# Kernel tuning notes

Measured on AMD Instinct MI355X. Metric: run time of the kernel, lower is better.

Reference implementation:

```python
import jax, jax.numpy as jnp
import numpy as np

N, D, H = 4096, 1024, 4096
EPS = 1e-5


def setup_inputs() -> dict:
    key = jax.random.key(0)
    ks = jax.random.split(key, 12)
    s_in = 1.0 / np.sqrt(D)
    s_hid = 1.0 / np.sqrt(H)
    return {
        "x": jax.random.normal(ks[0], (N, D), dtype=jnp.float32),
        "Wq": jax.random.uniform(ks[1], (D, H), jnp.float32, -s_in, s_in),
        "Wk": jax.random.uniform(ks[2], (D, H), jnp.float32, -s_in, s_in),
        "Wv": jax.random.uniform(ks[3], (D, H), jnp.float32, -s_in, s_in),
        "Wo": jax.random.uniform(ks[4], (H, D), jnp.float32, -s_hid, s_hid),
        "W1": jax.random.uniform(ks[5], (D, H), jnp.float32, -s_in, s_in),
        "b1": jax.random.uniform(ks[6], (H,), jnp.float32, -s_in, s_in),
        "W2": jax.random.uniform(ks[7], (H, D), jnp.float32, -s_hid, s_hid),
        "b2": jax.random.uniform(ks[8], (D,), jnp.float32, -s_hid, s_hid),
        "g1": jnp.ones((D,), jnp.float32),
        "be1": jnp.zeros((D,), jnp.float32),
        "g2": jnp.ones((D,), jnp.float32),
        "be2": jnp.zeros((D,), jnp.float32),
    }


def _layernorm(x, g, b):
    mu = jnp.mean(x, axis=-1, keepdims=True)
    var = jnp.mean(jnp.square(x - mu), axis=-1, keepdims=True)
    return (x - mu) * jax.lax.rsqrt(var + EPS) * g + b


def reference(x, Wq, Wk, Wv, Wo, W1, b1, W2, b2, g1, be1, g2, be2):
    # --- attention (single head, unscaled, as in the source) ---
    q = x @ Wq                      # [N, H]
    k = x @ Wk                      # [N, H]
    v = x @ Wv                      # [N, H]
    scores = jax.nn.softmax(q @ k.T, axis=-1)  # [N, N]
    attn = (scores @ v) @ Wo        # [N, D]
    h = _layernorm(x + attn, g1, be1)
    # --- feed-forward ---
    ff = jax.nn.relu(h @ W1 + b1) @ W2 + b2
    return _layernorm(h + ff, g2, be2)
```

## Files before the change

kernel.cpp:

```cpp
#include <hip/hip_runtime.h>
#include <hip/hip_bf16.h>

using f16 = _Float16;
typedef __attribute__((ext_vector_type(8))) f16 half8;
typedef __attribute__((ext_vector_type(4))) f16 half4;
typedef __attribute__((ext_vector_type(4))) float floatx4;

#define LN_EPS 1e-5f

__device__ __forceinline__ void gload_lds16(const f16* g, f16* l) {
  __builtin_amdgcn_global_load_lds(
      (const __attribute__((address_space(1))) void*)g,
      (__attribute__((address_space(3))) void*)l, 16, 0, 0);
}

#define CFENCE asm volatile("" ::: "memory")
#define WAIT_VM(N) asm volatile("s_waitcnt vmcnt(" #N ")" ::: "memory")
#define BARRIER()                    \
  do {                               \
    CFENCE;                          \
    __builtin_amdgcn_s_barrier();    \
    CFENCE;                          \
  } while (0)

template <int EPI>
__device__ __forceinline__ void gemm256_core(
    const f16* __restrict__ A, const f16* __restrict__ B,
    f16* __restrict__ Cz, const float* __restrict__ bias,
    int lda, int ldb, int ldc, int kper, int kbeg, int bm, int bn,
    f16* smp) {
  const int t = threadIdx.x;
  const int wave = t >> 6, lane = t & 63;
  const int wm = (wave >> 2) << 7;
  const int wn = (wave & 3) << 6;
  const int lrow = lane & 15, lkc = lane >> 4;

  const int srow = lane >> 3;
  const int schunk = ((lane & 7) ^ srow) << 3;
  const f16* Ag = A + (size_t)(bm + wave * 16 + srow) * lda + kbeg + schunk;
  const f16* Bg = B + (size_t)(bn + wave * 16 + srow) * ldb + kbeg + schunk;

  const int co0 = ((lkc ^ (lrow & 7)) << 3);
  const int co1 = (((4 + lkc) ^ (lrow & 7)) << 3);

  floatx4 acc[8][4] = {};
  half8 af[4][2];
  half8 bf[2][2][2];

  auto STAGE = [&](int b, int tt, int h) {
    if (h < 2) {
      const f16* src = Ag + (size_t)(h * 128) * lda + tt * 64;
      f16* d = smp + (b * 2) * 16384 + h * 8192 + wave * 1024;
      gload_lds16(src, d);
      gload_lds16(src + (size_t)8 * lda, d + 512);
    } else {
      const f16* src = Bg + (size_t)((h - 2) * 128) * ldb + tt * 64;
      f16* d = smp + (b * 2 + 1) * 16384 + (h - 2) * 8192 + wave * 1024;
      gload_lds16(src, d);
      gload_lds16(src + (size_t)8 * ldb, d + 512);
    }
  };
  auto LDA = [&](int b, int qm) {
    const f16* base = smp + (b * 2) * 16384 + (wm + qm * 64 + lrow) * 64;
#pragma unroll
    for (int fm = 0; fm < 4; ++fm) {
      af[fm][0] = *(const half8*)(base + fm * (16 * 64) + co0);
      af[fm][1] = *(const half8*)(base + fm * (16 * 64) + co1);
    }
  };
  auto LDB = [&](int b, int qn) {
    const f16* base = smp + (b * 2 + 1) * 16384 + (wn + qn * 32 + lrow) * 64;
#pragma unroll
    for (int fn = 0; fn < 2; ++fn) {
      bf[qn][fn][0] = *(const half8*)(base + fn * (16 * 64) + co0);
      bf[qn][fn][1] = *(const half8*)(base + fn * (16 * 64) + co1);
    }
  };
  auto MFMAQ = [&](int qm, int qn) {
    __builtin_amdgcn_s_setprio(1);
#pragma unroll
    for (int kk = 0; kk < 2; ++kk)
#pragma unroll
      for (int fm = 0; fm < 4; ++fm)
#pragma unroll
        for (int fn = 0; fn < 2; ++fn)
          acc[qm * 4 + fm][qn * 2 + fn] =
              __builtin_amdgcn_mfma_f32_16x16x32_f16(
                  af[fm][kk], bf[qn][fn][kk], acc[qm * 4 + fm][qn * 2 + fn],
                  0, 0, 0);
    __builtin_amdgcn_s_setprio(0);
  };

  const int NT = kper >> 6;
  const int NI = NT >> 1;

  STAGE(0, 0, 0); STAGE(0, 0, 1); STAGE(0, 0, 2); STAGE(0, 0, 3);
  STAGE(1, 1, 0);
  WAIT_VM(2);
  BARRIER();

  for (int i = 0; i < NI; ++i) {
    const bool last = (i == NI - 1);
    const int tb = 2 * i;
    LDA(0, 0); LDB(0, 0); STAGE(1, tb + 1, 1);
    BARRIER(); MFMAQ(0, 0); BARRIER();
    LDB(0, 1); STAGE(1, tb + 1, 2);
    BARRIER(); MFMAQ(0, 1); BARRIER();
    LDA(0, 1); STAGE(1, tb + 1, 3);
    BARRIER(); MFMAQ(1, 0); BARRIER();
    if (!last) {
      STAGE(0, tb + 2, 0);
      WAIT_VM(2);
    } else {
      WAIT_VM(0);
    }
    BARRIER(); MFMAQ(1, 1); BARRIER();
    LDA(1, 0); LDB(1, 0);
    if (!last) STAGE(0, tb + 2, 1);
    BARRIER(); MFMAQ(0, 0); BARRIER();
    LDB(1, 1);
    if (!last) STAGE(0, tb + 2, 2);
    BARRIER(); MFMAQ(0, 1); BARRIER();
    LDA(1, 1);
    if (!last) STAGE(0, tb + 2, 3);
    BARRIER(); MFMAQ(1, 0); BARRIER();
    if (!last) {
      STAGE(1, tb + 3, 0);
      WAIT_VM(2);
    }
    BARRIER(); MFMAQ(1, 1); BARRIER();
  }

  const int crow0 = bm + wm + lkc * 4;
  const int ccol0 = bn + wn + lrow;
#pragma unroll
  for (int i = 0; i < 8; ++i) {
#pragma unroll
    for (int r2 = 0; r2 < 4; ++r2) {
      const size_t row = (size_t)(crow0 + i * 16 + r2);
#pragma unroll
      for (int j = 0; j < 4; ++j) {
        const int col = ccol0 + j * 16;
        float v = acc[i][j][r2];
        if (EPI == 2) v = fmaxf(v + bias[col], 0.0f);
        Cz[row * (size_t)ldc + col] = (f16)v;
      }
    }
  }
}

__device__ __forceinline__ int xcd_swizzle(int id, int nwg) {
  const int q = nwg >> 3, r = nwg & 7;
  const int xcd = id & 7, lin = id >> 3;
  return (xcd < r ? xcd * (q + 1) : r * (q + 1) + (xcd - r) * q) + lin;
}

template <int EPI>
__global__ __launch_bounds__(512, 2) void gemm_nt256(
    const f16* __restrict__ A, const f16* __restrict__ B,
    f16* __restrict__ Ch, const float* __restrict__ bias,
    int M, int Nc, int K, int lda, int ldb, int ldc) {
  __shared__ f16 sm[4][256 * 64];
  const int gx = gridDim.x, gy = gridDim.y;
  const int nwg = gx * gy * gridDim.z;
  const int id = blockIdx.x + gx * (blockIdx.y + gy * blockIdx.z);
  const int nid = xcd_swizzle(id, nwg);
  const int bx = nid % gx;
  const int by = (nid / gx) % gy;
  const int bz = nid / (gx * gy);
  const int kper = K / gridDim.z;
  gemm256_core<EPI>(A, B, Ch + (size_t)bz * M * ldc, bias, lda, ldb, ldc,
                    kper, bz * kper, by << 8, bx << 8, &sm[0][0]);
}

__global__ __launch_bounds__(512, 2) void gemm_pre256(
    const f16* __restrict__ Wkb, const f16* __restrict__ Wqb,
    const f16* __restrict__ WoT, const f16* __restrict__ Wvb,
    f16* __restrict__ parQK, f16* __restrict__ parVO, int D, int H) {
  __shared__ f16 sm[4][256 * 64];
  const int id = blockIdx.x + 4 * (blockIdx.y + 4 * blockIdx.z);
  const int nid = xcd_swizzle(id, 256);
  const int bx = nid & 3, by = (nid >> 2) & 3, z = nid >> 4;
  const int zz = z & 7;
  const f16* A = (z < 8) ? Wkb : WoT;
  const f16* B = (z < 8) ? Wqb : Wvb;
  f16* slab = ((z < 8) ? parQK : parVO) + (size_t)zz * D * D;
  gemm256_core<1>(A, B, slab, nullptr, H, H, D, H / 8, zz * (H / 8),
                  by << 8, bx << 8, &sm[0][0]);
}

__global__ __launch_bounds__(512, 2) void gemm_dual256(
    const f16* __restrict__ xb, const f16* __restrict__ WqkT,
    const f16* __restrict__ WvoT, f16* __restrict__ th,
    f16* __restrict__ xvoT, int N, int D) {
  __shared__ f16 sm[4][256 * 64];
  const int id = blockIdx.x + 4 * blockIdx.y;
  const int nid = xcd_swizzle(id, 128);
  const int bx = nid & 3, y = nid >> 2;
  if (y < 16)
    gemm256_core<1>(xb, WqkT, th, nullptr, D, D, D, D, 0,
                    y << 8, bx << 8, &sm[0][0]);
  else
    gemm256_core<1>(WvoT, xb, xvoT, nullptr, D, D, N, D, 0,
                    bx << 8, (y - 16) << 8, &sm[0][0]);
}

__global__ void prep_inputs(const float* x, const float* Wq, const float* Wk,
                            const float* Wv, const float* W1, const float* Wo,
                            const float* W2, f16* xb, f16* Wqb, f16* Wkb,
                            f16* Wvb, f16* W1T, f16* WoT, f16* W2T) {
  const int z = blockIdx.y;
  const int b = blockIdx.x;
  const int t = threadIdx.x;
  if (z >= 3) {
    const float* in = (z == 3) ? x : (z == 4) ? Wq : (z == 5) ? Wk : Wv;
    f16* out = (z == 3) ? xb : (z == 4) ? Wqb : (z == 5) ? Wkb : Wvb;
    const size_t i = ((size_t)b * 256 + t) * 16;
    const float4 a0 = *(const float4*)(in + i);
    const float4 a1 = *(const float4*)(in + i + 4);
    const float4 a2 = *(const float4*)(in + i + 8);
    const float4 a3 = *(const float4*)(in + i + 12);
    half8 v0 = {(f16)a0.x, (f16)a0.y, (f16)a0.z, (f16)a0.w,
                (f16)a1.x, (f16)a1.y, (f16)a1.z, (f16)a1.w};
    half8 v1 = {(f16)a2.x, (f16)a2.y, (f16)a2.z, (f16)a2.w,
                (f16)a3.x, (f16)a3.y, (f16)a3.z, (f16)a3.w};
    *(half8*)(out + i) = v0;
    *(half8*)(out + i + 8) = v1;
    return;
  }
  int R, C, tx, ty;
  const float* in;
  f16* out;
  if (z == 0) {
    R = 1024; C = 4096; in = W1; out = W1T;
    tx = b & 63; ty = b >> 6;
  } else {
    R = 4096; C = 1024; in = (z == 1) ? Wo : W2;
    out = (z == 1) ? WoT : W2T;
    tx = b & 15; ty = b >> 4;
  }
  const int r0 = ty << 6, c0 = tx << 6;
  __shared__ f16 lt[64 * 64];
  const int lr = t >> 4;
  const int lc = t & 15;
  const int q3 = lr & 3;
  const int rb = lr & ~3;
  const int myc = lc * 4 + q3;
#pragma unroll
  for (int rr = 0; rr < 4; ++rr) {
    const int r = lr + rr * 16;
    const float4 f = *(const float4*)(in + (size_t)(r0 + r) * C + c0 + lc * 4);
    float v0 = f.x, v1 = f.y, v2 = f.z, v3 = f.w;
    {
      const bool hi = (q3 & 2) != 0;
      float sA = hi ? v0 : v2;
      float sB = hi ? v1 : v3;
      sA = __shfl_xor(sA, 32);
      sB = __shfl_xor(sB, 32);
      if (hi) { v0 = sA; v1 = sB; } else { v2 = sA; v3 = sB; }
    }
    {
      const bool od = (q3 & 1) != 0;
      float sC = od ? v0 : v1;
      float sD = od ? v2 : v3;
      sC = __shfl_xor(sC, 16);
      sD = __shfl_xor(sD, 16);
      if (od) { v0 = sC; v2 = sD; } else { v1 = sC; v3 = sD; }
    }
    half4 hv = {(f16)v0, (f16)v1, (f16)v2, (f16)v3};
    const int rbase = rb + rr * 16;
    *(half4*)(lt + myc * 64 + (rbase ^ ((myc & 15) << 2))) = hv;
  }
  __syncthreads();
  const int oc = t >> 3, orr = (t & 7) << 3;
#pragma unroll
  for (int cc = 0; cc < 2; ++cc) {
    const int c = oc + cc * 32;
    const int swz = (c & 15) << 2;
    const half4 ha = *(const half4*)(lt + c * 64 + (orr ^ swz));
    const half4 hb4 = *(const half4*)(lt + c * 64 + ((orr + 4) ^ swz));
    half8 v = {ha[0], ha[1], ha[2], ha[3], hb4[0], hb4[1], hb4[2], hb4[3]};
    *(half8*)(out + (size_t)(c0 + c) * R + r0 + orr) = v;
  }
}

__global__ void reduce_dual(const f16* __restrict__ parQK,
                            const f16* __restrict__ parVO,
                            f16* __restrict__ WqkT, f16* __restrict__ WvoT,
                            int n) {
  const int half = gridDim.x >> 1;
  const bool second = blockIdx.x >= half;
  const f16* par = second ? parVO : parQK;
  f16* out = second ? WvoT : WqkT;
  const int b = second ? blockIdx.x - half : blockIdx.x;
  const int i = (b * 256 + threadIdx.x) * 4;
  float s0 = 0, s1 = 0, s2 = 0, s3 = 0;
#pragma unroll
  for (int z = 0; z < 8; ++z) {
    const half4 p = *(const half4*)(par + (size_t)z * n + i);
    s0 += (float)p[0]; s1 += (float)p[1]; s2 += (float)p[2]; s3 += (float)p[3];
  }
  half4 o = {(f16)s0, (f16)s1, (f16)s2, (f16)s3};
  *(half4*)(out + i) = o;
}

__global__ void softmax_rows(const f16* __restrict__ S, f16* __restrict__ P,
                             int N) {
  const int row = blockIdx.x;
  const int t = threadIdx.x;
  const int lane = t & 63, wave = t >> 6;
  const f16* s = S + (size_t)row * N;
  const half8 a = *(const half8*)(s + t * 8);
  const half8 b = *(const half8*)(s + 2048 + t * 8);
  float v[16];
#pragma unroll
  for (int i = 0; i < 8; ++i) {
    v[i] = (float)a[i];
    v[8 + i] = (float)b[i];
  }
  float mx = -1e30f;
#pragma unroll
  for (int i = 0; i < 16; ++i) mx = fmaxf(mx, v[i]);
#pragma unroll
  for (int off = 32; off > 0; off >>= 1) mx = fmaxf(mx, __shfl_xor(mx, off));
  __shared__ float red[8];
  if (lane == 0) red[wave] = mx;
  __syncthreads();
  mx = fmaxf(fmaxf(red[0], red[1]), fmaxf(red[2], red[3]));
  float sum = 0.0f;
#pragma unroll
  for (int i = 0; i < 16; ++i) {
    v[i] = __expf(v[i] - mx);
    sum += v[i];
  }
#pragma unroll
  for (int off = 32; off > 0; off >>= 1) sum += __shfl_xor(sum, off);
  if (lane == 0) red[4 + wave] = sum;
  __syncthreads();
  const float inv = 1.0f / (red[4] + red[5] + red[6] + red[7]);
  f16* p = P + (size_t)row * N;
  half8 oa, ob;
#pragma unroll
  for (int i = 0; i < 8; ++i) {
    oa[i] = (f16)(v[i] * inv);
    ob[i] = (f16)(v[8 + i] * inv);
  }
  *(half8*)(p + t * 8) = oa;
  *(half8*)(p + 2048 + t * 8) = ob;
}

__global__ void add_ln(const float* __restrict__ a, const f16* __restrict__ b,
                       int nchunks, size_t cs, const float* __restrict__ bias,
                       const float* __restrict__ g, const float* __restrict__ be,
                       float* __restrict__ outf, f16* __restrict__ outh, int D) {
  const int row = blockIdx.x;
  const int t = threadIdx.x;
  const int lane = t & 63, wave = t >> 6;
  const float4 av = *(const float4*)(a + (size_t)row * D + t * 4);
  float s[4] = {av.x, av.y, av.z, av.w};
  for (int c = 0; c < nchunks; ++c) {
    const half4 bv = *(const half4*)(b + c * cs + (size_t)row * D + t * 4);
    s[0] += (float)bv[0]; s[1] += (float)bv[1];
    s[2] += (float)bv[2]; s[3] += (float)bv[3];
  }
  if (bias != nullptr) {
    const float4 bb = *(const float4*)(bias + t * 4);
    s[0] += bb.x; s[1] += bb.y; s[2] += bb.z; s[3] += bb.w;
  }
  float sum = s[0] + s[1] + s[2] + s[3];
  float sq = s[0] * s[0] + s[1] * s[1] + s[2] * s[2] + s[3] * s[3];
#pragma unroll
  for (int off = 32; off > 0; off >>= 1) {
    sum += __shfl_xor(sum, off);
    sq += __shfl_xor(sq, off);
  }
  __shared__ float red[8];
  if (lane == 0) {
    red[wave] = sum;
    red[4 + wave] = sq;
  }
  __syncthreads();
  sum = red[0] + red[1] + red[2] + red[3];
  sq = red[4] + red[5] + red[6] + red[7];
  const float mu = sum / (float)D;
  const float rv = rsqrtf(sq / (float)D - mu * mu + LN_EPS);
  const float4 gv = *(const float4*)(g + t * 4);
  const float4 bev = *(const float4*)(be + t * 4);
  float y0 = (s[0] - mu) * rv * gv.x + bev.x;
  float y1 = (s[1] - mu) * rv * gv.y + bev.y;
  float y2 = (s[2] - mu) * rv * gv.z + bev.z;
  float y3 = (s[3] - mu) * rv * gv.w + bev.w;
  if (outf != nullptr) {
    float4 o = {y0, y1, y2, y3};
    *(float4*)(outf + (size_t)row * D + t * 4) = o;
  }
  if (outh != nullptr) {
    f16* ob = outh + (size_t)row * D + t * 4;
    ob[0] = (f16)y0;
    ob[1] = (f16)y1;
    ob[2] = (f16)y2;
    ob[3] = (f16)y3;
  }
}

extern "C" void kernel_launch(void* const* d_in, const int* in_sizes, int n_in,
                              void* d_out, int out_size, void* d_ws,
                              size_t ws_size, hipStream_t stream) {
  constexpr int N = 4096, D = 1024, H = 4096;
  const float* x = (const float*)d_in[0];
  const float* Wq = (const float*)d_in[1];
  const float* Wk = (const float*)d_in[2];
  const float* Wv = (const float*)d_in[3];
  const float* Wo = (const float*)d_in[4];
  const float* W1 = (const float*)d_in[5];
  const float* b1 = (const float*)d_in[6];
  const float* W2 = (const float*)d_in[7];
  const float* b2 = (const float*)d_in[8];
  const float* g1 = (const float*)d_in[9];
  const float* be1 = (const float*)d_in[10];
  const float* g2 = (const float*)d_in[11];
  const float* be2 = (const float*)d_in[12];
  float* out = (float*)d_out;

  const size_t MB = 1024ull * 1024ull;
  char* w = (char*)d_ws;
  f16* xb   = (f16*)(w + 0 * MB);
  f16* Wqb  = (f16*)(w + 8 * MB);
  f16* Wkb  = (f16*)(w + 16 * MB);
  f16* Wvb  = (f16*)(w + 24 * MB);
  f16* WoT  = (f16*)(w + 32 * MB);
  f16* W1T  = (f16*)(w + 40 * MB);
  f16* W2T  = (f16*)(w + 48 * MB);
  f16* WqkT = (f16*)(w + 56 * MB);
  f16* WvoT = (f16*)(w + 58 * MB);
  f16* th   = (f16*)(w + 60 * MB);
  f16* xvoT = (f16*)(w + 68 * MB);
  f16* F1   = (f16*)(w + 76 * MB);
  f16* Sh   = (f16*)(w + 108 * MB);
  f16* parA = (f16*)(w + 108 * MB);
  f16* Pb   = (f16*)(w + 140 * MB);
  float* hf = (float*)(w + 172 * MB);
  f16* hb   = (f16*)(w + 188 * MB);
  f16* parQK = (f16*)(w + 196 * MB);
  f16* parVO = (f16*)(w + 212 * MB);

  prep_inputs<<<dim3(1024, 7), 256, 0, stream>>>(
      x, Wq, Wk, Wv, W1, Wo, W2, xb, Wqb, Wkb, Wvb, W1T, WoT, W2T);

  gemm_pre256<<<dim3(4, 4, 16), 512, 0, stream>>>(
      Wkb, Wqb, WoT, Wvb, parQK, parVO, D, H);
  reduce_dual<<<2 * (D * D) / 1024, 256, 0, stream>>>(parQK, parVO, WqkT,
                                                      WvoT, D * D);

  gemm_dual256<<<dim3(4, 32), 512, 0, stream>>>(xb, WqkT, WvoT, th, xvoT,
                                                N, D);
  gemm_nt256<1><<<dim3(N / 256, N / 256, 1), 512, 0, stream>>>(
      th, xb, Sh, nullptr, N, N, D, D, D, N);
  softmax_rows<<<N, 256, 0, stream>>>(Sh, Pb, N);
  gemm_nt256<1><<<dim3(D / 256, N / 256, 4), 512, 0, stream>>>(
      Pb, xvoT, parA, nullptr, N, D, N, N, N, D);
  add_ln<<<N, 256, 0, stream>>>(x, parA, 4, (size_t)N * D, nullptr, g1, be1,
                                hf, hb, D);

  gemm_nt256<2><<<dim3(H / 256, N / 256, 1), 512, 0, stream>>>(
      hb, W1T, F1, b1, N, H, D, D, D, H);
  gemm_nt256<1><<<dim3(D / 256, N / 256, 4), 512, 0, stream>>>(
      F1, W2T, parA, nullptr, N, D, H, H, H, D);
  add_ln<<<N, 256, 0, stream>>>(hf, parA, 4, (size_t)N * D, b2, g2, be2,
                                out, nullptr, D);
}
```

Measured before the change: 404.4 us.

## Fuse softmax into QK epilogue and PV GEMM A-operand staging

The standalone softmax kernel is removed. The QK^T GEMM epilogue now writes per-64-column partial row max and sum-of-exp values, a small kernel reduces these into per-row (max, 1/sum), and a new PV GEMM loads raw scores through registers, applies exp and normalization, and writes the result to LDS instead of using direct global-to-LDS loads. This drops one full N×N read and write pass. In exchange the PV GEMM does register staging plus exp work in its main loop, and the QK epilogue does extra shuffles. reduce_dual is also widened to 8-element vectors.

```diff
diff --git a/kernel.cpp b/kernel.cpp
--- a/kernel.cpp
+++ b/kernel.cpp
@@ -16,6 +16,11 @@
 
 #define CFENCE asm volatile("" ::: "memory")
 #define WAIT_VM(N) asm volatile("s_waitcnt vmcnt(" #N ")" ::: "memory")
+#define WAIT_LGKM0                                     \
+  do {                                                 \
+    asm volatile("s_waitcnt lgkmcnt(0)" ::: "memory"); \
+    __builtin_amdgcn_sched_barrier(0);                 \
+  } while (0)
 #define BARRIER()                    \
   do {                               \
     CFENCE;                          \
@@ -28,7 +33,7 @@
     const f16* __restrict__ A, const f16* __restrict__ B,
     f16* __restrict__ Cz, const float* __restrict__ bias,
     int lda, int ldb, int ldc, int kper, int kbeg, int bm, int bn,
-    f16* smp) {
+    f16* smp, float* __restrict__ Smax, float* __restrict__ Ssum) {
   const int t = threadIdx.x;
   const int wave = t >> 6, lane = t & 63;
   const int wm = (wave >> 2) << 7;
@@ -147,6 +152,29 @@
       }
     }
   }
+  if (EPI == 3) {
+    const int chunk = (bn + wn) >> 6;
+#pragma unroll
+    for (int i = 0; i < 8; ++i) {
+#pragma unroll
+      for (int r2 = 0; r2 < 4; ++r2) {
+        float mx = fmaxf(fmaxf(acc[i][0][r2], acc[i][1][r2]),
+                         fmaxf(acc[i][2][r2], acc[i][3][r2]));
+#pragma unroll
+        for (int m_ = 8; m_ >= 1; m_ >>= 1) mx = fmaxf(mx, __shfl_xor(mx, m_));
+        float s = 0.0f;
+#pragma unroll
+        for (int j = 0; j < 4; ++j) s += __expf(acc[i][j][r2] - mx);
+#pragma unroll
+        for (int m_ = 8; m_ >= 1; m_ >>= 1) s += __shfl_xor(s, m_);
+        if (lrow == 0) {
+          const int row = crow0 + i * 16 + r2;
+          Smax[(size_t)row * 64 + chunk] = mx;
+          Ssum[(size_t)row * 64 + chunk] = s;
+        }
+      }
+    }
+  }
 }
 
 __device__ __forceinline__ int xcd_swizzle(int id, int nwg) {
@@ -159,6 +187,7 @@
 __global__ __launch_bounds__(512, 2) void gemm_nt256(
     const f16* __restrict__ A, const f16* __restrict__ B,
     f16* __restrict__ Ch, const float* __restrict__ bias,
+    float* __restrict__ Smax, float* __restrict__ Ssum,
     int M, int Nc, int K, int lda, int ldb, int ldc) {
   __shared__ f16 sm[4][256 * 64];
   const int gx = gridDim.x, gy = gridDim.y;
@@ -170,7 +199,7 @@
   const int bz = nid / (gx * gy);
   const int kper = K / gridDim.z;
   gemm256_core<EPI>(A, B, Ch + (size_t)bz * M * ldc, bias, lda, ldb, ldc,
-                    kper, bz * kper, by << 8, bx << 8, &sm[0][0]);
+                    kper, bz * kper, by << 8, bx << 8, &sm[0][0], Smax, Ssum);
 }
 
 __global__ __launch_bounds__(512, 2) void gemm_pre256(
@@ -186,7 +215,7 @@
   const f16* B = (z < 8) ? Wqb : Wvb;
   f16* slab = ((z < 8) ? parQK : parVO) + (size_t)zz * D * D;
   gemm256_core<1>(A, B, slab, nullptr, H, H, D, H / 8, zz * (H / 8),
-                  by << 8, bx << 8, &sm[0][0]);
+                  by << 8, bx << 8, &sm[0][0], nullptr, nullptr);
 }
 
 __global__ __launch_bounds__(512, 2) void gemm_dual256(
@@ -199,10 +228,184 @@
   const int bx = nid & 3, y = nid >> 2;
   if (y < 16)
     gemm256_core<1>(xb, WqkT, th, nullptr, D, D, D, D, 0,
-                    y << 8, bx << 8, &sm[0][0]);
+                    y << 8, bx << 8, &sm[0][0], nullptr, nullptr);
   else
     gemm256_core<1>(WvoT, xb, xvoT, nullptr, D, D, N, D, 0,
-                    bx << 8, (y - 16) << 8, &sm[0][0]);
+                    bx << 8, (y - 16) << 8, &sm[0][0], nullptr, nullptr);
+}
+
+__global__ __launch_bounds__(512, 2) void gemm_pv256(
+    const f16* __restrict__ A, const f16* __restrict__ B,
+    f16* __restrict__ Ch, const float2* __restrict__ rowstat,
+    int M, int Nc, int K, int lda, int ldb, int ldc) {
+  __shared__ f16 sm[4][256 * 64];
+  f16* smp = &sm[0][0];
+  const int gx = gridDim.x, gy = gridDim.y;
+  const int nwg = gx * gy * gridDim.z;
+  const int id = blockIdx.x + gx * (blockIdx.y + gy * blockIdx.z);
+  const int nid = xcd_swizzle(id, nwg);
+  const int bx = nid % gx;
+  const int by = (nid / gx) % gy;
+  const int bz = nid / (gx * gy);
+  const int kper = K / gridDim.z;
+  const int kbeg = bz * kper;
+  f16* Cz = Ch + (size_t)bz * M * ldc;
+  const int bm = by << 8, bn = bx << 8;
+
+  const int t = threadIdx.x;
+  const int wave = t >> 6, lane = t & 63;
+  const int wm = (wave >> 2) << 7;
+  const int wn = (wave & 3) << 6;
+  const int lrow = lane & 15, lkc = lane >> 4;
+  const int srow = lane >> 3;
+  const int schunk = ((lane & 7) ^ srow) << 3;
+  const f16* Ag = A + (size_t)(bm + wave * 16 + srow) * lda + kbeg + schunk;
+  const f16* Bg = B + (size_t)(bn + wave * 16 + srow) * ldb + kbeg + schunk;
+  const int co0 = ((lkc ^ (lrow & 7)) << 3);
+  const int co1 = (((4 + lkc) ^ (lrow & 7)) << 3);
+
+  const int r0s = bm + wave * 16 + srow;
+  const float2 st00 = rowstat[r0s], st01 = rowstat[r0s + 8];
+  const float2 st10 = rowstat[r0s + 128], st11 = rowstat[r0s + 136];
+
+  floatx4 acc[8][4] = {};
+  half8 af[4][2];
+  half8 bf[2][2][2];
+  half8 pCa, pCb, p0a, p0b, p1a, p1b;
+
+  auto ALOAD = [&](int tt, int h, half8& ra, half8& rb) {
+    const f16* src = Ag + (size_t)(h * 128) * lda + tt * 64;
+    ra = *(const half8*)(src);
+    rb = *(const half8*)(src + (size_t)8 * lda);
+  };
+  auto AWRITE = [&](int b, int h, const half8& ra, const half8& rb,
+                    const float2& sa, const float2& sb) {
+    f16* d = smp + (b * 2) * 16384 + h * 8192 + wave * 1024 + lane * 8;
+    half8 oa, ob;
+#pragma unroll
+    for (int k = 0; k < 8; ++k) {
+      oa[k] = (f16)(__expf((float)ra[k] - sa.x) * sa.y);
+      ob[k] = (f16)(__expf((float)rb[k] - sb.x) * sb.y);
+    }
+    *(half8*)d = oa;
+    *(half8*)(d + 512) = ob;
+  };
+  auto BSTAGE = [&](int b, int tt, int h) {
+    const f16* src = Bg + (size_t)((h - 2) * 128) * ldb + tt * 64;
+    f16* d = smp + (b * 2 + 1) * 16384 + (h - 2) * 8192 + wave * 1024;
+    gload_lds16(src, d);
+    gload_lds16(src + (size_t)8 * ldb, d + 512);
+  };
+  auto LDA = [&](int b, int qm) {
+    const f16* base = smp + (b * 2) * 16384 + (wm + qm * 64 + lrow) * 64;
+#pragma unroll
+    for (int fm = 0; fm < 4; ++fm) {
+      af[fm][0] = *(const half8*)(base + fm * (16 * 64) + co0);
+      af[fm][1] = *(const half8*)(base + fm * (16 * 64) + co1);
+    }
+  };
+  auto LDB = [&](int b, int qn) {
+    const f16* base = smp + (b * 2 + 1) * 16384 + (wn + qn * 32 + lrow) * 64;
+#pragma unroll
+    for (int fn = 0; fn < 2; ++fn) {
+      bf[qn][fn][0] = *(const half8*)(base + fn * (16 * 64) + co0);
+      bf[qn][fn][1] = *(const half8*)(base + fn * (16 * 64) + co1);
+    }
+  };
+  auto MFMAQ = [&](int qm, int qn) {
+    __builtin_amdgcn_s_setprio(1);
+#pragma unroll
+    for (int kk = 0; kk < 2; ++kk)
+#pragma unroll
+      for (int fm = 0; fm < 4; ++fm)
+#pragma unroll
+        for (int fn = 0; fn < 2; ++fn)
+          acc[qm * 4 + fm][qn * 2 + fn] =
+              __builtin_amdgcn_mfma_f32_16x16x32_f16(
+                  af[fm][kk], bf[qn][fn][kk], acc[qm * 4 + fm][qn * 2 + fn],
+                  0, 0, 0);
+    __builtin_amdgcn_s_setprio(0);
+  };
+
+  const int NT = kper >> 6;
+  const int NI = NT >> 1;
+
+  ALOAD(0, 0, pCa, pCb);
+  ALOAD(0, 1, p1a, p1b);
+  BSTAGE(0, 0, 2); BSTAGE(0, 0, 3);
+  ALOAD(1, 0, p0a, p0b);
+  WAIT_VM(2);
+  AWRITE(0, 0, pCa, pCb, st00, st01);
+  AWRITE(0, 1, p1a, p1b, st10, st11);
+  WAIT_LGKM0;
+  BARRIER();
+
+  for (int i = 0; i < NI; ++i) {
+    const bool last = (i == NI - 1);
+    const int tb = 2 * i;
+    LDA(0, 0); LDB(0, 0); ALOAD(tb + 1, 1, p1a, p1b);
+    BARRIER(); MFMAQ(0, 0); BARRIER();
+    LDB(0, 1); BSTAGE(1, tb + 1, 2);
+    BARRIER(); MFMAQ(0, 1); BARRIER();
+    LDA(0, 1); BSTAGE(1, tb + 1, 3);
+    BARRIER(); MFMAQ(1, 0); BARRIER();
+    if (!last) {
+      ALOAD(tb + 2, 0, pCa, pCb);
+      WAIT_VM(2);
+    } else {
+      WAIT_VM(0);
+    }
+    AWRITE(1, 0, p0a, p0b, st00, st01);
+    AWRITE(1, 1, p1a, p1b, st10, st11);
+    WAIT_LGKM0;
+    BARRIER(); MFMAQ(1, 1); BARRIER();
+    LDA(1, 0); LDB(1, 0);
+    if (!last) ALOAD(tb + 2, 1, p1a, p1b);
+    BARRIER(); MFMAQ(0, 0); BARRIER();
+    LDB(1, 1);
+    if (!last) BSTAGE(0, tb + 2, 2);
+    BARRIER(); MFMAQ(0, 1); BARRIER();
+    LDA(1, 1);
+    if (!last) BSTAGE(0, tb + 2, 3);
+    BARRIER(); MFMAQ(1, 0); BARRIER();
+    if (!last) {
+      ALOAD(tb + 3, 0, p0a, p0b);
+      WAIT_VM(2);
+      AWRITE(0, 0, pCa, pCb, st00, st01);
+      AWRITE(0, 1, p1a, p1b, st10, st11);
+      WAIT_LGKM0;
+    }
+    BARRIER(); MFMAQ(1, 1); BARRIER();
+  }
+
+  const int crow0 = bm + wm + lkc * 4;
+  const int ccol0 = bn + wn + lrow;
+#pragma unroll
+  for (int i = 0; i < 8; ++i) {
+#pragma unroll
+    for (int r2 = 0; r2 < 4; ++r2) {
+      const size_t row = (size_t)(crow0 + i * 16 + r2);
+#pragma unroll
+      for (int j = 0; j < 4; ++j)
+        Cz[row * (size_t)ldc + ccol0 + j * 16] = (f16)acc[i][j][r2];
+    }
+  }
+}
+
+__global__ void smax_reduce(const float* __restrict__ Smax,
+                            const float* __restrict__ Ssum,
+                            float2* __restrict__ rowstat) {
+  const int row = blockIdx.x * 4 + (threadIdx.x >> 6);
+  const int c = threadIdx.x & 63;
+  const float mp = Smax[(size_t)row * 64 + c];
+  const float sp = Ssum[(size_t)row * 64 + c];
+  float m = mp;
+#pragma unroll
+  for (int off = 32; off > 0; off >>= 1) m = fmaxf(m, __shfl_xor(m, off));
+  float s = sp * __expf(mp - m);
+#pragma unroll
+  for (int off = 32; off > 0; off >>= 1) s += __shfl_xor(s, off);
+  if (c == 0) rowstat[row] = make_float2(m, 1.0f / s);
 }
 
 __global__ void prep_inputs(const float* x, const float* Wq, const float* Wk,
@@ -293,60 +496,17 @@
   const f16* par = second ? parVO : parQK;
   f16* out = second ? WvoT : WqkT;
   const int b = second ? blockIdx.x - half : blockIdx.x;
-  const int i = (b * 256 + threadIdx.x) * 4;
-  float s0 = 0, s1 = 0, s2 = 0, s3 = 0;
+  const int i = (b * 256 + threadIdx.x) * 8;
+  float s[8] = {};
 #pragma unroll
   for (int z = 0; z < 8; ++z) {
-    const half4 p = *(const half4*)(par + (size_t)z * n + i);
-    s0 += (float)p[0]; s1 += (float)p[1]; s2 += (float)p[2]; s3 += (float)p[3];
-  }
-  half4 o = {(f16)s0, (f16)s1, (f16)s2, (f16)s3};
-  *(half4*)(out + i) = o;
-}
-
-__global__ void softmax_rows(const f16* __restrict__ S, f16* __restrict__ P,
-                             int N) {
-  const int row = blockIdx.x;
-  const int t = threadIdx.x;
-  const int lane = t & 63, wave = t >> 6;
-  const f16* s = S + (size_t)row * N;
-  const half8 a = *(const half8*)(s + t * 8);
-  const half8 b = *(const half8*)(s + 2048 + t * 8);
-  float v[16];
-#pragma unroll
-  for (int i = 0; i < 8; ++i) {
-    v[i] = (float)a[i];
-    v[8 + i] = (float)b[i];
-  }
-  float mx = -1e30f;
-#pragma unroll
-  for (int i = 0; i < 16; ++i) mx = fmaxf(mx, v[i]);
-#pragma unroll
-  for (int off = 32; off > 0; off >>= 1) mx = fmaxf(mx, __shfl_xor(mx, off));
-  __shared__ float red[8];
-  if (lane == 0) red[wave] = mx;
-  __syncthreads();
-  mx = fmaxf(fmaxf(red[0], red[1]), fmaxf(red[2], red[3]));
-  float sum = 0.0f;
-#pragma unroll
-  for (int i = 0; i < 16; ++i) {
-    v[i] = __expf(v[i] - mx);
-    sum += v[i];
-  }
-#pragma unroll
-  for (int off = 32; off > 0; off >>= 1) sum += __shfl_xor(sum, off);
-  if (lane == 0) red[4 + wave] = sum;
-  __syncthreads();
-  const float inv = 1.0f / (red[4] + red[5] + red[6] + red[7]);
-  f16* p = P + (size_t)row * N;
-  half8 oa, ob;
-#pragma unroll
-  for (int i = 0; i < 8; ++i) {
-    oa[i] = (f16)(v[i] * inv);
-    ob[i] = (f16)(v[8 + i] * inv);
-  }
-  *(half8*)(p + t * 8) = oa;
-  *(half8*)(p + 2048 + t * 8) = ob;
+    const half8 p = *(const half8*)(par + (size_t)z * n + i);
+#pragma unroll
+    for (int k = 0; k < 8; ++k) s[k] += (float)p[k];
+  }
+  half8 o = {(f16)s[0], (f16)s[1], (f16)s[2], (f16)s[3],
+             (f16)s[4], (f16)s[5], (f16)s[6], (f16)s[7]};
+  *(half8*)(out + i) = o;
 }
 
 __global__ void add_ln(const float* __restrict__ a, const f16* __restrict__ b,
@@ -437,35 +597,37 @@
   f16* xvoT = (f16*)(w + 68 * MB);
   f16* F1   = (f16*)(w + 76 * MB);
   f16* Sh   = (f16*)(w + 108 * MB);
-  f16* parA = (f16*)(w + 108 * MB);
-  f16* Pb   = (f16*)(w + 140 * MB);
+  f16* parA = (f16*)(w + 140 * MB);
   float* hf = (float*)(w + 172 * MB);
   f16* hb   = (f16*)(w + 188 * MB);
   f16* parQK = (f16*)(w + 196 * MB);
   f16* parVO = (f16*)(w + 212 * MB);
+  float* Smax = (float*)(w + 196 * MB);
+  float* Ssum = (float*)(w + 197 * MB);
+  float2* rowstat = (float2*)(w + 198 * MB);
 
   prep_inputs<<<dim3(1024, 7), 256, 0, stream>>>(
       x, Wq, Wk, Wv, W1, Wo, W2, xb, Wqb, Wkb, Wvb, W1T, WoT, W2T);
 
   gemm_pre256<<<dim3(4, 4, 16), 512, 0, stream>>>(
       Wkb, Wqb, WoT, Wvb, parQK, parVO, D, H);
-  reduce_dual<<<2 * (D * D) / 1024, 256, 0, stream>>>(parQK, parVO, WqkT,
+  reduce_dual<<<2 * (D * D) / 2048, 256, 0, stream>>>(parQK, parVO, WqkT,
                                                       WvoT, D * D);
 
   gemm_dual256<<<dim3(4, 32), 512, 0, stream>>>(xb, WqkT, WvoT, th, xvoT,
                                                 N, D);
-  gemm_nt256<1><<<dim3(N / 256, N / 256, 1), 512, 0, stream>>>(
-      th, xb, Sh, nullptr, N, N, D, D, D, N);
-  softmax_rows<<<N, 256, 0, stream>>>(Sh, Pb, N);
-  gemm_nt256<1><<<dim3(D / 256, N / 256, 4), 512, 0, stream>>>(
-      Pb, xvoT, parA, nullptr, N, D, N, N, N, D);
+  gemm_nt256<3><<<dim3(N / 256, N / 256, 1), 512, 0, stream>>>(
+      th, xb, Sh, nullptr, Smax, Ssum, N, N, D, D, D, N);
+  smax_reduce<<<N / 4, 256, 0, stream>>>(Smax, Ssum, rowstat);
+  gemm_pv256<<<dim3(D / 256, N / 256, 4), 512, 0, stream>>>(
+      Sh, xvoT, parA, rowstat, N, D, N, N, N, D);
   add_ln<<<N, 256, 0, stream>>>(x, parA, 4, (size_t)N * D, nullptr, g1, be1,
                                 hf, hb, D);
 
   gemm_nt256<2><<<dim3(H / 256, N / 256, 1), 512, 0, stream>>>(
-      hb, W1T, F1, b1, N, H, D, D, D, H);
+      hb, W1T, F1, b1, nullptr, nullptr, N, H, D, D, D, H);
   gemm_nt256<1><<<dim3(D / 256, N / 256, 4), 512, 0, stream>>>(
-      F1, W2T, parA, nullptr, N, D, H, H, H, D);
+      F1, W2T, parA, nullptr, nullptr, nullptr, N, D, H, H, H, D);
   add_ln<<<N, 256, 0, stream>>>(hf, parA, 4, (size_t)N * D, b2, g2, be2,
                                 out, nullptr, D);
 }
```

After: 491.0 us. +21.4%, slower.
